# Kernel optimization log

Hardware: AMD Instinct MI355X
Metric: run time of the kernel (lower is better)

## Reference

```python
import jax, jax.numpy as jnp
import numpy as np

B, S, E = 2, 2048, 2048
H, KV, D = 8, 4, 256
WIN = 1024          # sliding window
EPS = 1e-6          # rms_norm_eps
ROPE_THETA = 10000.0


def _rope_tables(key):
    inv_freq = 1.0 / (ROPE_THETA ** (jnp.arange(0, D, 2, dtype=jnp.float32) / D))
    pos = jnp.arange(S, dtype=jnp.float32)
    freqs = pos[:, None] * inv_freq[None, :]            # [S, D/2]
    emb = jnp.concatenate([freqs, freqs], axis=-1)      # [S, D]
    cos = jnp.broadcast_to(jnp.cos(emb)[None], (B, S, D))
    sin = jnp.broadcast_to(jnp.sin(emb)[None], (B, S, D))
    return cos, sin


def setup_inputs() -> dict:
    key = jax.random.key(0)
    ks = jax.random.split(key, 8)
    hidden_states = jax.random.normal(ks[0], (B, S, E), dtype=jnp.float32)
    cos, sin = _rope_tables(ks[1])
    attention_mask = jnp.ones((B, S), dtype=jnp.int32)
    std = 0.02
    Wq = jax.random.normal(ks[2], (E, H * D), dtype=jnp.float32) * std
    Wk = jax.random.normal(ks[3], (E, KV * D), dtype=jnp.float32) * std
    Wv = jax.random.normal(ks[4], (E, KV * D), dtype=jnp.float32) * std
    Wo = jax.random.normal(ks[5], (H * D, E), dtype=jnp.float32) * std
    q_norm_w = jnp.zeros((D,), dtype=jnp.float32)  # weight init is zeros; scale = 1 + w
    k_norm_w = jnp.zeros((D,), dtype=jnp.float32)
    return {"hidden_states": hidden_states, "cos": cos, "sin": sin,
            "attention_mask": attention_mask, "Wq": Wq, "Wk": Wk, "Wv": Wv,
            "Wo": Wo, "q_norm_w": q_norm_w, "k_norm_w": k_norm_w}


def _rms_norm(x, w):
    # Gemma-style: x / rms(x) * (1 + w), variance in fp32
    var = jnp.mean(jnp.square(x.astype(jnp.float32)), axis=-1, keepdims=True)
    x = x / jnp.sqrt(var + EPS)
    return (1.0 + w) * x.astype(jnp.float32)


def _rotate_half(t):
    h = t.shape[-1] // 2
    return jnp.concatenate([-t[..., h:], t[..., :h]], axis=-1)


def _apply_rope(t, sin, cos):
    # t: [B,S,h,D], sin/cos: [B,S,D]
    return t * cos[:, :, None, :] + _rotate_half(t) * sin[:, :, None, :]


def reference(hidden_states, cos, sin, attention_mask, Wq, Wk, Wv, Wo, q_norm_w, k_norm_w):
    b, s, _ = hidden_states.shape
    q = (hidden_states @ Wq).reshape(b, s, H, D)
    k = (hidden_states @ Wk).reshape(b, s, KV, D)
    v = (hidden_states @ Wv).reshape(b, s, KV, D)

    q = _rms_norm(q, q_norm_w)
    k = _rms_norm(k, k_norm_w)
    q = _apply_rope(q, sin, cos)
    k = _apply_rope(k, sin, cos)

    # GQA: repeat KV heads
    groups = H // KV
    k = jnp.repeat(k, groups, axis=2)  # [b,s,H,D]
    v = jnp.repeat(v, groups, axis=2)

    scale = D ** -0.5
    scores = jnp.einsum('bqhd,bkhd->bhqk', q * scale, k)  # [b,H,s,s]

    # causal + sliding-window + padding mask
    i = jnp.arange(s)[:, None]
    j = jnp.arange(s)[None, :]
    band = (j <= i) & ((i - j) < WIN)                      # [s,s]
    pad = attention_mask[:, None, None, :] > 0             # [b,1,1,s]
    allowed = band[None, None] & pad
    neg = jnp.finfo(scores.dtype).min
    bias = jnp.where(allowed, 0.0, neg).astype(scores.dtype)

    attn = jax.nn.softmax(scores + bias, axis=-1)
    out = jnp.einsum('bhqk,bkhd->bqhd', attn, v).reshape(b, s, H * D)
    return out @ Wo
```

## Files before the change

### kernel.cpp

```cpp
#include <hip/hip_runtime.h>
#include <math.h>

#define BB   2
#define SS   2048
#define EE   2048
#define HH   8
#define KVN  4
#define DD   256
#define WINW 1024
#define EPSV 1e-6f
#define NQKV 4096

using bf16x8 = __attribute__((ext_vector_type(8))) __bf16;
using f32x4  = __attribute__((ext_vector_type(4))) float;

__device__ __forceinline__ unsigned short f2bf(float f) {
    union { float f; unsigned int u; } c; c.f = f;
    unsigned int u = c.u;
    unsigned int r = (u + 0x7FFFu + ((u >> 16) & 1u)) >> 16;
    return (unsigned short)r;
}
__device__ __forceinline__ float bf2f(unsigned short u) {
    union { unsigned int u; float f; } c; c.u = ((unsigned int)u) << 16;
    return c.f;
}

#if defined(__has_builtin)
#if __has_builtin(__builtin_amdgcn_global_load_lds)
#define HAVE_GLL 1
#endif
#endif

#ifdef HAVE_GLL
#define GLOAD_LDS16(gp, sp) __builtin_amdgcn_global_load_lds( \
    (const __attribute__((address_space(1))) unsigned int*)(gp), \
    (__attribute__((address_space(3))) unsigned int*)(sp), 16, 0, 0)
#endif

__global__ __launch_bounds__(256)
void conv_x(const float* __restrict__ X, unsigned short* __restrict__ Xb)
{
    const size_t i = ((size_t)blockIdx.x * 256 + threadIdx.x) * 8;
    const float4 a = *(const float4*)(X + i);
    const float4 b = *(const float4*)(X + i + 4);
    ushort4 lo, hi;
    lo.x = f2bf(a.x); lo.y = f2bf(a.y); lo.z = f2bf(a.z); lo.w = f2bf(a.w);
    hi.x = f2bf(b.x); hi.y = f2bf(b.y); hi.z = f2bf(b.z); hi.w = f2bf(b.w);
    *(ushort4*)(Xb + i)     = lo;
    *(ushort4*)(Xb + i + 4) = hi;
}

__global__ __launch_bounds__(256)
void conv_wt(const float* __restrict__ Wq, const float* __restrict__ Wk,
             const float* __restrict__ Wv, unsigned short* __restrict__ Wt)
{
    __shared__ unsigned short Lt[64][72];
    const int k0 = blockIdx.x * 64, n0 = blockIdx.y * 64;
    const int t = threadIdx.x;
    const float* src; int ld, nc;
    if (n0 < 2048)      { src = Wq; ld = 2048; nc = n0; }
    else if (n0 < 3072) { src = Wk; ld = 1024; nc = n0 - 2048; }
    else                { src = Wv; ld = 1024; nc = n0 - 3072; }

#pragma unroll
    for (int p = 0; p < 4; ++p) {
        const int kr = p * 16 + (t >> 4);
        const float4 fv = *(const float4*)(src + (size_t)(k0 + kr) * ld + nc + (t & 15) * 4);
        Lt[kr][(t & 15) * 4 + 0] = f2bf(fv.x);
        Lt[kr][(t & 15) * 4 + 1] = f2bf(fv.y);
        Lt[kr][(t & 15) * 4 + 2] = f2bf(fv.z);
        Lt[kr][(t & 15) * 4 + 3] = f2bf(fv.w);
    }
    __syncthreads();
    const int n = t >> 2, kseg = t & 3;
    unsigned short tmp[16];
#pragma unroll
    for (int j = 0; j < 16; ++j) tmp[j] = Lt[kseg * 16 + j][n];
    unsigned short* dst = Wt + (size_t)(n0 + n) * EE + k0 + kseg * 16;
    *(uint4*)(dst)     = *(uint4*)&tmp[0];
    *(uint4*)(dst + 8) = *(uint4*)&tmp[8];
}

__global__ __launch_bounds__(256)
void conv_wo(const float* __restrict__ W, unsigned short* __restrict__ Wot)
{
    __shared__ unsigned short Lt[64][72];
    const int k0 = blockIdx.x * 64, n0 = blockIdx.y * 64;
    const int t = threadIdx.x;

#pragma unroll
    for (int p = 0; p < 4; ++p) {
        const int kr = p * 16 + (t >> 4);
        const float4 fv = *(const float4*)(W + (size_t)(k0 + kr) * 2048 + n0 + (t & 15) * 4);
        Lt[kr][(t & 15) * 4 + 0] = f2bf(fv.x);
        Lt[kr][(t & 15) * 4 + 1] = f2bf(fv.y);
        Lt[kr][(t & 15) * 4 + 2] = f2bf(fv.z);
        Lt[kr][(t & 15) * 4 + 3] = f2bf(fv.w);
    }
    __syncthreads();
    const int n = t >> 2, kseg = t & 3;
    unsigned short tmp[16];
#pragma unroll
    for (int j = 0; j < 16; ++j) tmp[j] = Lt[kseg * 16 + j][n];
    unsigned short* dst = Wot + (size_t)(n0 + n) * 2048 + k0 + kseg * 16;
    *(uint4*)(dst)     = *(uint4*)&tmp[0];
    *(uint4*)(dst + 8) = *(uint4*)&tmp[8];
}

template <bool F32OUT>
__global__ __launch_bounds__(256)
void gemm_bf16(const unsigned short* __restrict__ A,
               const unsigned short* __restrict__ Bt,
               void* __restrict__ Cv, int M, int N, int K)
{
    __shared__ unsigned short As[128 * 32];
    __shared__ unsigned short Bs[128 * 32];
    const int t = threadIdx.x;
    const int w = t >> 6;
    const int l = t & 63;
    const int bm = blockIdx.y * 128, bn = blockIdx.x * 128;
    const int wr = w >> 1, wc = w & 1;
    const int l16 = l & 15, lq = l >> 4;

    const int srow = t >> 2;
    const int sk8  = (t & 3) * 8;
    const unsigned short* Ag = A  + (size_t)(bm + srow) * K + sk8;
    const unsigned short* Bg = Bt + (size_t)(bn + srow) * K + sk8;

    f32x4 acc[4][4];
#pragma unroll
    for (int i = 0; i < 4; ++i)
#pragma unroll
        for (int j = 0; j < 4; ++j) acc[i][j] = (f32x4){0.f, 0.f, 0.f, 0.f};

    for (int k0 = 0; k0 < K; k0 += 32) {
        __syncthreads();
#ifdef HAVE_GLL
        GLOAD_LDS16(Ag + k0,            &As[t * 8]);
        GLOAD_LDS16(Ag + k0 + 64 * K,   &As[2048 + t * 8]);
        GLOAD_LDS16(Bg + k0,            &Bs[t * 8]);
        GLOAD_LDS16(Bg + k0 + 64 * K,   &Bs[2048 + t * 8]);
#else
        const uint4 a0 = *(const uint4*)(Ag + k0);
        const uint4 a1 = *(const uint4*)(Ag + k0 + 64 * K);
        const uint4 b0 = *(const uint4*)(Bg + k0);
        const uint4 b1 = *(const uint4*)(Bg + k0 + 64 * K);
        *(uint4*)&As[t * 8]        = a0;
        *(uint4*)&As[2048 + t * 8] = a1;
        *(uint4*)&Bs[t * 8]        = b0;
        *(uint4*)&Bs[2048 + t * 8] = b1;
#endif
        __syncthreads();

        bf16x8 af[4], bf[4];
#pragma unroll
        for (int i = 0; i < 4; ++i)
            af[i] = *(const bf16x8*)&As[(wr * 64 + i * 16 + l16) * 32 + lq * 8];
#pragma unroll
        for (int j = 0; j < 4; ++j)
            bf[j] = *(const bf16x8*)&Bs[(wc * 64 + j * 16 + l16) * 32 + lq * 8];
#pragma unroll
        for (int i = 0; i < 4; ++i)
#pragma unroll
            for (int j = 0; j < 4; ++j)
                acc[i][j] = __builtin_amdgcn_mfma_f32_16x16x32_bf16(af[i], bf[j], acc[i][j], 0, 0, 0);
    }

#pragma unroll
    for (int i = 0; i < 4; ++i)
#pragma unroll
        for (int j = 0; j < 4; ++j)
#pragma unroll
            for (int r = 0; r < 4; ++r) {
                const size_t idx = (size_t)(bm + wr * 64 + i * 16 + lq * 4 + r) * N +
                                   (bn + wc * 64 + j * 16 + l16);
                if constexpr (F32OUT) ((float*)Cv)[idx] = acc[i][j][r];
                else ((unsigned short*)Cv)[idx] = f2bf(acc[i][j][r]);
            }
}

template <int NH, int COLOFF>
__global__ __launch_bounds__(256)
void rmsnorm_rope_qkv(const unsigned short* __restrict__ qkv,
                      unsigned short* __restrict__ out,
                      const float* __restrict__ w,
                      const float* __restrict__ cs, const float* __restrict__ sn,
                      float scale)
{
    const int wv   = threadIdx.x >> 6;
    const int lane = threadIdx.x & 63;
    const int row  = blockIdx.x * 4 + wv;
    const int m    = row / NH;
    const int hh   = row - m * NH;
    const unsigned short* xr = qkv + (size_t)m * NQKV + COLOFF + hh * DD;

    const ushort4 u4 = ((const ushort4*)xr)[lane];
    float4 xv;
    xv.x = bf2f(u4.x); xv.y = bf2f(u4.y); xv.z = bf2f(u4.z); xv.w = bf2f(u4.w);
    float ss = xv.x * xv.x + xv.y * xv.y + xv.z * xv.z + xv.w * xv.w;
#pragma unroll
    for (int d = 1; d < 64; d <<= 1) ss += __shfl_xor(ss, d, 64);
    const float inv = 1.0f / sqrtf(ss * (1.0f / (float)DD) + EPSV);

    const float4 w4 = ((const float4*)w)[lane];
    float4 y;
    y.x = xv.x * inv * (1.f + w4.x);
    y.y = xv.y * inv * (1.f + w4.y);
    y.z = xv.z * inv * (1.f + w4.z);
    y.w = xv.w * inv * (1.f + w4.w);

    __shared__ float4 buf[4][64];
    buf[wv][lane] = y;
    __syncthreads();
    const float4 r0 = buf[wv][(lane < 32) ? (lane + 32) : (lane - 32)];
    float4 rot;
    if (lane < 32) { rot.x = -r0.x; rot.y = -r0.y; rot.z = -r0.z; rot.w = -r0.w; }
    else           { rot = r0; }

    const float4 c4 = ((const float4*)(cs + (size_t)m * DD))[lane];
    const float4 s4 = ((const float4*)(sn + (size_t)m * DD))[lane];
    ushort4 o4;
    o4.x = f2bf((y.x * c4.x + rot.x * s4.x) * scale);
    o4.y = f2bf((y.y * c4.y + rot.y * s4.y) * scale);
    o4.z = f2bf((y.z * c4.z + rot.z * s4.z) * scale);
    o4.w = f2bf((y.w * c4.w + rot.w * s4.w) * scale);
    ((ushort4*)(out + (size_t)row * DD))[lane] = o4;
}

__global__ __launch_bounds__(256)
void v_to_vt(const unsigned short* __restrict__ qkv, unsigned short* __restrict__ Vt)
{
    __shared__ unsigned short Lt[64][72];
    const int s0 = blockIdx.x * 64, d0 = blockIdx.y * 64;
    const int bkv = blockIdx.z;
    const int b = bkv >> 2, kv = bkv & 3;
    const int t = threadIdx.x;

    {
        const int s = t >> 2, seg = t & 3;
        const unsigned short* src = qkv + (size_t)(b * SS + s0 + s) * NQKV +
                                    3072 + kv * DD + d0 + seg * 16;
        *(uint4*)&Lt[s][seg * 16]     = *(const uint4*)(src);
        *(uint4*)&Lt[s][seg * 16 + 8] = *(const uint4*)(src + 8);
    }
    __syncthreads();
    {
        const int d = t >> 2, sseg = t & 3;
        unsigned short tmp[16];
#pragma unroll
        for (int j = 0; j < 16; ++j) tmp[j] = Lt[sseg * 16 + j][d];
        unsigned short* dst = Vt + ((size_t)bkv * DD + d0 + d) * SS + s0 + sseg * 16;
        *(uint4*)(dst)     = *(uint4*)&tmp[0];
        *(uint4*)(dst + 8) = *(uint4*)&tmp[8];
    }
}

__global__ __launch_bounds__(256, 2)
void attn_mfma(const unsigned short* __restrict__ Qb,
               const unsigned short* __restrict__ Kb,
               const unsigned short* __restrict__ Vt,
               const int* __restrict__ am, unsigned short* __restrict__ O)
{
    __shared__ unsigned short Ks[32 * 256];
    __shared__ unsigned short Vts[256 * 32];
    __shared__ unsigned short Pl[4][16 * 40];
    __shared__ int Ams[32];

    const int t = threadIdx.x, w = t >> 6, l = t & 63;
    const int g = l >> 4, q15 = l & 15;
    const int qb0 = blockIdx.x * 64, h = blockIdx.y, b = blockIdx.z;
    const int kvh = h >> 1;
    const int qrow = qb0 + w * 16 + q15;

    bf16x8 qf[8];
    {
        const unsigned short* qp = Qb + ((size_t)(b * SS + qrow) * HH + h) * DD + g * 8;
#pragma unroll
        for (int km = 0; km < 8; ++km) qf[km] = *(const bf16x8*)(qp + km * 32);
    }

    f32x4 oacc[16];
#pragma unroll
    for (int i = 0; i < 16; ++i) oacc[i] = (f32x4){0.f, 0.f, 0.f, 0.f};
    float mrow = -1e30f, lrow = 0.f;

    const int qlo = qb0 + w * 16, qhi = qlo + 15;
    int kstart = qb0 - 1024; if (kstart < 0) kstart = 0;
    const int kend = qb0 + 32;

    const int sj = t >> 3, sc = t & 7;

    for (int k0 = kstart; k0 <= kend; k0 += 32) {
        {
            const unsigned short* kp = Kb + ((size_t)(b * SS + k0 + sj) * KVN + kvh) * DD + sc * 32;
#pragma unroll
            for (int i = 0; i < 4; ++i) {
                const int cc = sc * 4 + i;
                *(uint4*)&Ks[sj * 256 + ((cc ^ (sj & 7)) * 8)] = *(const uint4*)(kp + i * 8);
            }
#pragma unroll
            for (int it = 0; it < 4; ++it) {
                const int d = it * 64 + (t >> 2), c = t & 3;
                const unsigned short* vp = Vt + ((size_t)(b * KVN + kvh) * DD + d) * SS + k0 + c * 8;
                *(uint4*)&Vts[d * 32 + ((c ^ (d & 3)) * 8)] = *(const uint4*)vp;
            }
            if (t < 32) Ams[t] = am[b * SS + k0 + t];
        }
        __syncthreads();

        if (k0 <= qhi && k0 + 31 >= qlo - (WINW - 1)) {
            float pv[8];
            int   okf[8];
            float tmax = -1e30f;
#pragma unroll
            for (int jb = 0; jb < 2; ++jb) {
                f32x4 sacc = (f32x4){0.f, 0.f, 0.f, 0.f};
                const int krow = jb * 16 + q15;
                const unsigned short* kbase = &Ks[krow * 256];
                const int kx = krow & 7;
#pragma unroll
                for (int km = 0; km < 8; ++km) {
                    const bf16x8 kf = *(const bf16x8*)(kbase + (((km * 4 + g) ^ kx) * 8));
                    sacc = __builtin_amdgcn_mfma_f32_16x16x32_bf16(kf, qf[km], sacc, 0, 0, 0);
                }
#pragma unroll
                for (int r = 0; r < 4; ++r) {
                    const int jgl = k0 + jb * 16 + g * 4 + r;
                    const bool ok = (jgl <= qrow) && (qrow - jgl < WINW) &&
                                    (Ams[jb * 16 + g * 4 + r] != 0);
                    const float val = ok ? sacc[r] : -1e30f;
                    okf[jb * 4 + r] = ok;
                    pv[jb * 4 + r] = val;
                    tmax = fmaxf(tmax, val);
                }
            }
            tmax = fmaxf(tmax, __shfl_xor(tmax, 16, 64));
            tmax = fmaxf(tmax, __shfl_xor(tmax, 32, 64));
            const float mnew = fmaxf(mrow, tmax);
            const float corr = __expf(mrow - mnew);
            float ps = 0.f;
#pragma unroll
            for (int i = 0; i < 8; ++i) {
                const float p = okf[i] ? __expf(pv[i] - mnew) : 0.f;
                pv[i] = p; ps += p;
            }
            ps += __shfl_xor(ps, 16, 64);
            ps += __shfl_xor(ps, 32, 64);
            lrow = lrow * corr + ps;
            mrow = mnew;

            unsigned short* Pw = &Pl[w][0];
#pragma unroll
            for (int jb = 0; jb < 2; ++jb) {
                const unsigned int u0 = (unsigned int)f2bf(pv[jb * 4 + 0]) |
                                        ((unsigned int)f2bf(pv[jb * 4 + 1]) << 16);
                const unsigned int u1 = (unsigned int)f2bf(pv[jb * 4 + 2]) |
                                        ((unsigned int)f2bf(pv[jb * 4 + 3]) << 16);
                *(unsigned int*)&Pw[q15 * 40 + jb * 16 + g * 4]     = u0;
                *(unsigned int*)&Pw[q15 * 40 + jb * 16 + g * 4 + 2] = u1;
            }

            if (__any(corr != 1.0f)) {
                const float c0 = __shfl(corr, g * 4 + 0, 64);
                const float c1 = __shfl(corr, g * 4 + 1, 64);
                const float c2 = __shfl(corr, g * 4 + 2, 64);
                const float c3 = __shfl(corr, g * 4 + 3, 64);
#pragma unroll
                for (int dm = 0; dm < 16; ++dm) {
                    oacc[dm][0] *= c0; oacc[dm][1] *= c1;
                    oacc[dm][2] *= c2; oacc[dm][3] *= c3;
                }
            }

            asm volatile("s_waitcnt lgkmcnt(0)" ::: "memory");
            const bf16x8 pa = *(const bf16x8*)&Pw[q15 * 40 + g * 8];
#pragma unroll
            for (int dm = 0; dm < 16; ++dm) {
                const int d = dm * 16 + q15;
                const bf16x8 vf = *(const bf16x8*)&Vts[d * 32 + ((g ^ (d & 3)) * 8)];
                oacc[dm] = __builtin_amdgcn_mfma_f32_16x16x32_bf16(pa, vf, oacc[dm], 0, 0, 0);
            }
        }
        __syncthreads();
    }

    float invl[4];
#pragma unroll
    for (int r = 0; r < 4; ++r) invl[r] = 1.0f / __shfl(lrow, g * 4 + r, 64);
#pragma unroll
    for (int dm = 0; dm < 16; ++dm) {
#pragma unroll
        for (int r = 0; r < 4; ++r) {
            const int qo = qb0 + w * 16 + g * 4 + r;
            O[((size_t)(b * SS + qo) * HH + h) * DD + dm * 16 + q15] =
                f2bf(oacc[dm][r] * invl[r]);
        }
    }
}

extern "C" void kernel_launch(void* const* d_in, const int* in_sizes, int n_in,
                              void* d_out, int out_size, void* d_ws, size_t ws_size,
                              hipStream_t stream)
{
    (void)in_sizes; (void)n_in; (void)out_size; (void)ws_size;

    const float* X  = (const float*)d_in[0];
    const float* cs = (const float*)d_in[1];
    const float* sn = (const float*)d_in[2];
    const int*   am = (const int*)d_in[3];
    const float* Wq = (const float*)d_in[4];
    const float* Wk = (const float*)d_in[5];
    const float* Wv = (const float*)d_in[6];
    const float* Wo = (const float*)d_in[7];
    const float* qw = (const float*)d_in[8];
    const float* kw = (const float*)d_in[9];
    float* out = (float*)d_out;

    char* ws = (char*)d_ws;
    unsigned short* Xb  = (unsigned short*)(ws);
    unsigned short* Qb  = (unsigned short*)(ws);
    unsigned short* Wt  = (unsigned short*)(ws + (size_t)16 * 1024 * 1024);
    unsigned short* Kb  = (unsigned short*)(ws + (size_t)16 * 1024 * 1024);
    unsigned short* Vt  = (unsigned short*)(ws + (size_t)24 * 1024 * 1024);
    unsigned short* qkv = (unsigned short*)(ws + (size_t)32 * 1024 * 1024);
    unsigned short* Wot = (unsigned short*)(ws + (size_t)32 * 1024 * 1024);
    unsigned short* Ob  = (unsigned short*)(ws + (size_t)40 * 1024 * 1024);

    const int M = BB * SS;
    dim3 blk(256);

    conv_x <<<dim3((M * EE) / (256 * 8)), blk, 0, stream>>>(X, Xb);
    conv_wt<<<dim3(EE / 64, NQKV / 64), blk, 0, stream>>>(Wq, Wk, Wv, Wt);

    gemm_bf16<false><<<dim3(NQKV / 128, M / 128), blk, 0, stream>>>(Xb, Wt, qkv, M, NQKV, EE);

    rmsnorm_rope_qkv<KVN, 2048><<<dim3(M * KVN / 4), blk, 0, stream>>>(qkv, Kb, kw, cs, sn, 1.0f);
    rmsnorm_rope_qkv<HH, 0>    <<<dim3(M * HH  / 4), blk, 0, stream>>>(qkv, Qb, qw, cs, sn, 0.0625f);
    v_to_vt<<<dim3(SS / 64, DD / 64, BB * KVN), blk, 0, stream>>>(qkv, Vt);

    conv_wo<<<dim3(2048 / 64, 2048 / 64), blk, 0, stream>>>(Wo, Wot);

    attn_mfma<<<dim3(SS / 64, HH, BB), blk, 0, stream>>>(Qb, Kb, Vt, am, Ob);

    gemm_bf16<true><<<dim3(EE / 128, M / 128), blk, 0, stream>>>(Ob, Wot, out, M, EE, EE);
}
```

Measured before the change: 450.9 us.

## Prefetch next K/V tile into registers in attention; swizzle GEMM block order

The attention loop now loads the next K, V and mask tile from global memory into registers while the current tile is being computed, then writes them to shared memory after a barrier. This hides global-load latency behind the MFMA work, at the cost of extra registers for the staged tile. The GEMM kernel also remaps workgroup IDs so that consecutive IDs are spread in groups of eight, which is meant to improve cache locality across the chip's dies (XCDs).

```diff
diff --git a/kernel.cpp b/kernel.cpp
--- a/kernel.cpp
+++ b/kernel.cpp
@@ -118,7 +118,14 @@
     const int t = threadIdx.x;
     const int w = t >> 6;
     const int l = t & 63;
-    const int bm = blockIdx.y * 128, bn = blockIdx.x * 128;
+
+    const int nbx = gridDim.x;
+    const int nwg = nbx * gridDim.y;
+    const int lid = blockIdx.y * nbx + blockIdx.x;
+    const int cpx = nwg >> 3;
+    const int sid = (lid & 7) * cpx + (lid >> 3);
+    const int bm = (sid / nbx) * 128, bn = (sid % nbx) * 128;
+
     const int wr = w >> 1, wc = w & 1;
     const int l16 = l & 15, lq = l >> 4;
 
@@ -289,24 +296,51 @@
     const int kend = qb0 + 32;
 
     const int sj = t >> 3, sc = t & 7;
+    const int vd0 = t >> 2, vc = t & 3;
+
+    uint4 kreg[4], vreg[4];
+    int amreg = 0;
+    const size_t kvbase = (size_t)(b * KVN + kvh);
+
+    {
+        const unsigned short* kp = Kb + ((size_t)(b * SS + kstart + sj) * KVN + kvh) * DD + sc * 32;
+#pragma unroll
+        for (int i = 0; i < 4; ++i) kreg[i] = *(const uint4*)(kp + i * 8);
+#pragma unroll
+        for (int it = 0; it < 4; ++it) {
+            const int d = it * 64 + vd0;
+            vreg[it] = *(const uint4*)(Vt + (kvbase * DD + d) * SS + kstart + vc * 8);
+        }
+        if (t < 32) amreg = am[b * SS + kstart + t];
+    }
+#pragma unroll
+    for (int i = 0; i < 4; ++i) {
+        const int cc = sc * 4 + i;
+        *(uint4*)&Ks[sj * 256 + ((cc ^ (sj & 7)) * 8)] = kreg[i];
+    }
+#pragma unroll
+    for (int it = 0; it < 4; ++it) {
+        const int d = it * 64 + vd0;
+        *(uint4*)&Vts[d * 32 + ((vc ^ (d & 3)) * 8)] = vreg[it];
+    }
+    if (t < 32) Ams[t] = amreg;
+    __syncthreads();
 
     for (int k0 = kstart; k0 <= kend; k0 += 32) {
-        {
-            const unsigned short* kp = Kb + ((size_t)(b * SS + k0 + sj) * KVN + kvh) * DD + sc * 32;
-#pragma unroll
-            for (int i = 0; i < 4; ++i) {
-                const int cc = sc * 4 + i;
-                *(uint4*)&Ks[sj * 256 + ((cc ^ (sj & 7)) * 8)] = *(const uint4*)(kp + i * 8);
-            }
+        const int kn = k0 + 32;
+        const bool hasNext = (kn <= kend);
+
+        if (hasNext) {
+            const unsigned short* kp = Kb + ((size_t)(b * SS + kn + sj) * KVN + kvh) * DD + sc * 32;
+#pragma unroll
+            for (int i = 0; i < 4; ++i) kreg[i] = *(const uint4*)(kp + i * 8);
 #pragma unroll
             for (int it = 0; it < 4; ++it) {
-                const int d = it * 64 + (t >> 2), c = t & 3;
-                const unsigned short* vp = Vt + ((size_t)(b * KVN + kvh) * DD + d) * SS + k0 + c * 8;
-                *(uint4*)&Vts[d * 32 + ((c ^ (d & 3)) * 8)] = *(const uint4*)vp;
-            }
-            if (t < 32) Ams[t] = am[b * SS + k0 + t];
+                const int d = it * 64 + vd0;
+                vreg[it] = *(const uint4*)(Vt + (kvbase * DD + d) * SS + kn + vc * 8);
+            }
+            if (t < 32) amreg = am[b * SS + kn + t];
         }
-        __syncthreads();
 
         if (k0 <= qhi && k0 + 31 >= qlo - (WINW - 1)) {
             float pv[8];
@@ -380,6 +414,21 @@
                 const bf16x8 vf = *(const bf16x8*)&Vts[d * 32 + ((g ^ (d & 3)) * 8)];
                 oacc[dm] = __builtin_amdgcn_mfma_f32_16x16x32_bf16(pa, vf, oacc[dm], 0, 0, 0);
             }
+        }
+        __syncthreads();
+
+        if (hasNext) {
+#pragma unroll
+            for (int i = 0; i < 4; ++i) {
+                const int cc = sc * 4 + i;
+                *(uint4*)&Ks[sj * 256 + ((cc ^ (sj & 7)) * 8)] = kreg[i];
+            }
+#pragma unroll
+            for (int it = 0; it < 4; ++it) {
+                const int d = it * 64 + vd0;
+                *(uint4*)&Vts[d * 32 + ((vc ^ (d & 3)) * 8)] = vreg[it];
+            }
+            if (t < 32) Ams[t] = amreg;
         }
         __syncthreads();
     }
```

After: 527.6 us. 1.17x slower.
